# Kernel optimization log

Measured on AMD Instinct MI355X. Metric: run time of the kernel, lower is better.

Reference implementation:

```python
import jax, jax.numpy as jnp
import numpy as np

W = 16          # hidden width
N_HIDDEN = 8    # number of 16->16 hidden layers (num_layers - 1)
N_PTS = 2097152


def setup_inputs() -> dict:
    key = jax.random.key(0)
    ks = jax.random.split(key, 7)
    x = jax.random.uniform(ks[0], (N_PTS, 3), dtype=jnp.float32) * 2.0 - 1.0
    # nn.init.normal_ -> std-normal weights; biases left at (small) values
    W0 = jax.random.normal(ks[1], (W, 3), dtype=jnp.float32)
    b0 = jnp.zeros((W,), dtype=jnp.float32)
    Wh = jax.random.normal(ks[2], (N_HIDDEN, W, W), dtype=jnp.float32)
    bh = jnp.zeros((N_HIDDEN, W), dtype=jnp.float32)
    Wo = jax.random.normal(ks[3], (1, W), dtype=jnp.float32)
    bo = jnp.zeros((1,), dtype=jnp.float32)
    return {"x": x, "W0": W0, "b0": b0, "Wh": Wh, "bh": bh, "Wo": Wo, "bo": bo}


def reference(x, W0, b0, Wh, bh, Wo, bo):
    # Linear(3,16) + tanh
    h = jnp.tanh(x @ W0.T + b0)                     # [N, 16]
    def step(h, wb):
        w, b = wb
        return jnp.tanh(h @ w.T + b), None
    h, _ = jax.lax.scan(step, h, (Wh, bh))
    # Linear(16,1) + sigmoid
    return jax.nn.sigmoid(h @ Wo.T + bo)            # [N, 1]
```

## Files before the change

kernel.cpp:

```cpp
#include <hip/hip_runtime.h>

typedef __attribute__((ext_vector_type(4))) _Float16 half4;
typedef __attribute__((ext_vector_type(8))) _Float16 half8;
typedef __attribute__((ext_vector_type(4))) float floatx4;
typedef __attribute__((ext_vector_type(4))) unsigned uint4v;

#define NH 8
#define CHUNKS 8

struct Split2 { unsigned hi, lo; };

__device__ __forceinline__ Split2 split2(float t0, float t1) {
    unsigned hp = __builtin_bit_cast(unsigned, __builtin_amdgcn_cvt_pkrtz(t0, t1));
    float h0 = (float)__builtin_bit_cast(_Float16, (unsigned short)(hp & 0xffffu));
    float h1 = (float)__builtin_bit_cast(_Float16, (unsigned short)(hp >> 16));
    float l0 = (t0 - h0) * 2048.0f;
    float l1 = (t1 - h1) * 2048.0f;
    Split2 r;
    r.hi = hp;
    r.lo = __builtin_bit_cast(unsigned, __builtin_amdgcn_cvt_pkrtz(l0, l1));
    return r;
}

__device__ __forceinline__ floatx4 quad_r(float s0, float s1, float s2, float s3) {
    s0 = fminf(s0, 25.0f); s1 = fminf(s1, 25.0f);
    s2 = fminf(s2, 25.0f); s3 = fminf(s3, 25.0f);
    float p0 = __builtin_amdgcn_exp2f(s0) + 1.0f;
    float p1 = __builtin_amdgcn_exp2f(s1) + 1.0f;
    float p2 = __builtin_amdgcn_exp2f(s2) + 1.0f;
    float p3 = __builtin_amdgcn_exp2f(s3) + 1.0f;
    float A = p0 * p1, B = p2 * p3;
    float P = A * B;
    float rp = __builtin_amdgcn_rcpf(P);
    float rA = rp * B, rB = rp * A;
    floatx4 r;
    r[0] = rA * p1; r[1] = rA * p0; r[2] = rB * p3; r[3] = rB * p2;
    return r;
}

__device__ __forceinline__ void split_w(float w, float& hi, float& lo) {
    _Float16 h = (_Float16)w;
    hi = (float)h;
    lo = (w - hi) * 2048.0f;
}

__device__ __forceinline__ half8 mk_frag(floatx4 rq) {
    Split2 p01 = split2(rq[0], rq[1]);
    Split2 p23 = split2(rq[2], rq[3]);
    uint4v hb;
    hb.x = p01.hi; hb.y = p23.hi;
    hb.z = p01.lo; hb.w = p23.lo;
    return __builtin_bit_cast(half8, hb);
}

__global__ __launch_bounds__(256, 4) void cppn_kernel(
    const float* __restrict__ x,
    const float* __restrict__ W0,
    const float* __restrict__ b0,
    const float* __restrict__ Wh,
    const float* __restrict__ bh,
    const float* __restrict__ Wo,
    const float* __restrict__ bo,
    float* __restrict__ out)
{
    const int tid  = threadIdx.x;
    const int lane = tid & 63;
    const int col  = lane & 15;
    const int kg   = lane >> 4;
    const int wib  = tid >> 6;

    const float TSCL = 2.8853900817779268f;
    const float NSCL = -2.0f * TSCL;
    const float OSCL = -1.4426950408889634f;
    const float UNSC = 4.8828125e-4f;

    half8   wA8[NH];
    floatx4 bC[NH];
    #pragma unroll
    for (int l = 0; l < NH; ++l) {
        const float* wrow = Wh + l*256 + col*16 + kg*4;
        float w0 = wrow[0], w1 = wrow[1], w2 = wrow[2], w3 = wrow[3];
        float rs = (w0 + w1) + (w2 + w3);
        rs += __shfl_xor(rs, 16);
        rs += __shfl_xor(rs, 32);
        float h0,h1,h2,h3, lo0,lo1,lo2,lo3;
        split_w(w0*NSCL, h0, lo0);
        split_w(w1*NSCL, h1, lo1);
        split_w(w2*NSCL, h2, lo2);
        split_w(w3*NSCL, h3, lo3);
        uint4v wa;
        wa.x = __builtin_bit_cast(unsigned, __builtin_amdgcn_cvt_pkrtz(lo0, lo1));
        wa.y = __builtin_bit_cast(unsigned, __builtin_amdgcn_cvt_pkrtz(lo2, lo3));
        wa.z = __builtin_bit_cast(unsigned, __builtin_amdgcn_cvt_pkrtz(h0, h1));
        wa.w = __builtin_bit_cast(unsigned, __builtin_amdgcn_cvt_pkrtz(h2, h3));
        wA8[l] = __builtin_bit_cast(half8, wa);
        floatx4 c;
        #pragma unroll
        for (int r = 0; r < 4; ++r) {
            float rs_r = __shfl(rs, kg*4 + r);
            c[r] = TSCL * (bh[l*16 + kg*4 + r] + rs_r);
        }
        bC[l] = c;
    }

    float w0r[4][3]; float b0r[4];
    #pragma unroll
    for (int r = 0; r < 4; ++r) {
        const float* wp = W0 + (kg*4 + r)*3;
        w0r[r][0] = wp[0]*TSCL; w0r[r][1] = wp[1]*TSCL; w0r[r][2] = wp[2]*TSCL;
        b0r[r] = b0[kg*4 + r]*TSCL;
    }

    float woP[4];
    float wsum;
    {
        const float* wp = Wo + kg*4;
        float a = wp[0], b = wp[1], c2 = wp[2], d = wp[3];
        wsum = (a + b) + (c2 + d);
        wsum += __shfl_xor(wsum, 16);
        wsum += __shfl_xor(wsum, 32);
        woP[0] = a*(-2.0f*OSCL); woP[1] = b*(-2.0f*OSCL);
        woP[2] = c2*(-2.0f*OSCL); woP[3] = d*(-2.0f*OSCL);
    }
    const float boP = OSCL * (bo[0] + wsum);

    const floatx4 zeroC = {0.0f, 0.0f, 0.0f, 0.0f};
    const int base0 = (blockIdx.x * 4 + wib) * (64 * CHUNKS);

    #pragma unroll 1
    for (int c = 0; c < CHUNKS; ++c) {
        const int base = base0 + c * 64;

        half8 hB[4];
        #pragma unroll
        for (int t = 0; t < 4; ++t) {
            const int p = base + t*16 + col;
            const float x0 = x[p*3+0], x1 = x[p*3+1], x2 = x[p*3+2];
            float a0 = fmaf(w0r[0][0],x0, fmaf(w0r[0][1],x1, fmaf(w0r[0][2],x2, b0r[0])));
            float a1 = fmaf(w0r[1][0],x0, fmaf(w0r[1][1],x1, fmaf(w0r[1][2],x2, b0r[1])));
            float a2 = fmaf(w0r[2][0],x0, fmaf(w0r[2][1],x1, fmaf(w0r[2][2],x2, b0r[2])));
            float a3 = fmaf(w0r[3][0],x0, fmaf(w0r[3][1],x1, fmaf(w0r[3][2],x2, b0r[3])));
            hB[t] = mk_frag(quad_r(a0, a1, a2, a3));
        }

        #pragma unroll
        for (int l = 0; l < NH-1; ++l) {
            const half8 wa8 = wA8[l];
            const half4 whi = __builtin_shufflevector(wa8, wa8, 4, 5, 6, 7);
            const floatx4 bc = bC[l];
            #pragma unroll
            for (int tp = 0; tp < 2; ++tp) {
                const int u0 = tp*2, u1 = tp*2+1;
                const half4 bhi0 = __builtin_shufflevector(hB[u0], hB[u0], 0, 1, 2, 3);
                const half4 bhi1 = __builtin_shufflevector(hB[u1], hB[u1], 0, 1, 2, 3);
                floatx4 d0 = __builtin_amdgcn_mfma_f32_16x16x16f16(whi, bhi0, bc, 0,0,0);
                floatx4 d1 = __builtin_amdgcn_mfma_f32_16x16x16f16(whi, bhi1, bc, 0,0,0);
                floatx4 e0 = __builtin_amdgcn_mfma_f32_16x16x32_f16(wa8, hB[u0], zeroC, 0,0,0);
                floatx4 e1 = __builtin_amdgcn_mfma_f32_16x16x32_f16(wa8, hB[u1], zeroC, 0,0,0);

                floatx4 q0 = quad_r(fmaf(e0[0], UNSC, d0[0]),
                                    fmaf(e0[1], UNSC, d0[1]),
                                    fmaf(e0[2], UNSC, d0[2]),
                                    fmaf(e0[3], UNSC, d0[3]));
                floatx4 q1 = quad_r(fmaf(e1[0], UNSC, d1[0]),
                                    fmaf(e1[1], UNSC, d1[1]),
                                    fmaf(e1[2], UNSC, d1[2]),
                                    fmaf(e1[3], UNSC, d1[3]));
                hB[u0] = mk_frag(q0);
                hB[u1] = mk_frag(q1);
            }
        }

        float tot[4];
        {
            const half8 wa8 = wA8[NH-1];
            const half4 whi = __builtin_shufflevector(wa8, wa8, 4, 5, 6, 7);
            const floatx4 bc = bC[NH-1];
            #pragma unroll
            for (int t = 0; t < 4; ++t) {
                const half4 bhi = __builtin_shufflevector(hB[t], hB[t], 0, 1, 2, 3);
                floatx4 d = __builtin_amdgcn_mfma_f32_16x16x16f16(whi, bhi, bc, 0,0,0);
                floatx4 e = __builtin_amdgcn_mfma_f32_16x16x32_f16(wa8, hB[t], zeroC, 0,0,0);
                floatx4 r8 = quad_r(fmaf(e[0], UNSC, d[0]),
                                    fmaf(e[1], UNSC, d[1]),
                                    fmaf(e[2], UNSC, d[2]),
                                    fmaf(e[3], UNSC, d[3]));
                float acc = fmaf(woP[0], r8[0],
                            fmaf(woP[1], r8[1],
                            fmaf(woP[2], r8[2], woP[3] * r8[3])));
                acc += __shfl_xor(acc, 16);
                acc += __shfl_xor(acc, 32);
                tot[t] = acc;
            }
        }

        float s = (kg == 0) ? tot[0] : (kg == 1) ? tot[1] : (kg == 2) ? tot[2] : tot[3];
        s += boP;
        float E = __builtin_amdgcn_exp2f(s);
        out[base + lane] = __builtin_amdgcn_rcpf(1.0f + E);
    }
}

extern "C" void kernel_launch(void* const* d_in, const int* in_sizes, int n_in,
                              void* d_out, int out_size, void* d_ws, size_t ws_size,
                              hipStream_t stream) {
    const float* x  = (const float*)d_in[0];
    const float* W0 = (const float*)d_in[1];
    const float* b0 = (const float*)d_in[2];
    const float* Wh = (const float*)d_in[3];
    const float* bh = (const float*)d_in[4];
    const float* Wo = (const float*)d_in[5];
    const float* bo = (const float*)d_in[6];
    float* out = (float*)d_out;

    int n = out_size;
    int block = 256;
    long ptsPerBlock = 4L * 64 * CHUNKS;
    int grid = (int)((n + ptsPerBlock - 1) / ptsPerBlock);
    cppn_kernel<<<grid, block, 0, stream>>>(x, W0, b0, Wh, bh, Wo, bo, out);
}
```

Before: 109.1 us.

## Stage preprocessed weights in LDS and cap VGPRs to raise occupancy

Result: faster. 100.2 us (-8.2%).

```diff
diff --git a/kernel.cpp b/kernel.cpp
--- a/kernel.cpp
+++ b/kernel.cpp
@@ -6,7 +6,7 @@
 typedef __attribute__((ext_vector_type(4))) unsigned uint4v;
 
 #define NH 8
-#define CHUNKS 8
+#define CHUNKS 4
 
 struct Split2 { unsigned hi, lo; };
 
@@ -53,7 +53,11 @@
     return __builtin_bit_cast(half8, hb);
 }
 
-__global__ __launch_bounds__(256, 4) void cppn_kernel(
+__global__ __launch_bounds__(256)
+#if __has_attribute(amdgpu_num_vgpr)
+__attribute__((amdgpu_num_vgpr(60)))
+#endif
+void cppn_kernel(
     const float* __restrict__ x,
     const float* __restrict__ W0,
     const float* __restrict__ b0,
@@ -63,6 +67,12 @@
     const float* __restrict__ bo,
     float* __restrict__ out)
 {
+    __shared__ uint4v  s_wA[NH][64];
+    __shared__ floatx4 s_bC[NH][4];
+    __shared__ floatx4 s_w0[4][4];
+    __shared__ floatx4 s_wo4[4];
+    __shared__ float   s_boP;
+
     const int tid  = threadIdx.x;
     const int lane = tid & 63;
     const int col  = lane & 15;
@@ -74,55 +84,52 @@
     const float OSCL = -1.4426950408889634f;
     const float UNSC = 4.8828125e-4f;
 
-    half8   wA8[NH];
-    floatx4 bC[NH];
-    #pragma unroll
-    for (int l = 0; l < NH; ++l) {
-        const float* wrow = Wh + l*256 + col*16 + kg*4;
-        float w0 = wrow[0], w1 = wrow[1], w2 = wrow[2], w3 = wrow[3];
-        float rs = (w0 + w1) + (w2 + w3);
-        rs += __shfl_xor(rs, 16);
-        rs += __shfl_xor(rs, 32);
-        float h0,h1,h2,h3, lo0,lo1,lo2,lo3;
-        split_w(w0*NSCL, h0, lo0);
-        split_w(w1*NSCL, h1, lo1);
-        split_w(w2*NSCL, h2, lo2);
-        split_w(w3*NSCL, h3, lo3);
-        uint4v wa;
-        wa.x = __builtin_bit_cast(unsigned, __builtin_amdgcn_cvt_pkrtz(lo0, lo1));
-        wa.y = __builtin_bit_cast(unsigned, __builtin_amdgcn_cvt_pkrtz(lo2, lo3));
-        wa.z = __builtin_bit_cast(unsigned, __builtin_amdgcn_cvt_pkrtz(h0, h1));
-        wa.w = __builtin_bit_cast(unsigned, __builtin_amdgcn_cvt_pkrtz(h2, h3));
-        wA8[l] = __builtin_bit_cast(half8, wa);
-        floatx4 c;
-        #pragma unroll
-        for (int r = 0; r < 4; ++r) {
-            float rs_r = __shfl(rs, kg*4 + r);
-            c[r] = TSCL * (bh[l*16 + kg*4 + r] + rs_r);
-        }
-        bC[l] = c;
+    if (tid < 64) {
+        #pragma unroll
+        for (int l = 0; l < NH; ++l) {
+            const float* wrow = Wh + l*256 + col*16 + kg*4;
+            float w0v = wrow[0], w1v = wrow[1], w2v = wrow[2], w3v = wrow[3];
+            float rs = (w0v + w1v) + (w2v + w3v);
+            rs += __shfl_xor(rs, 16);
+            rs += __shfl_xor(rs, 32);
+            float h0,h1,h2,h3, lo0,lo1,lo2,lo3;
+            split_w(w0v*NSCL, h0, lo0);
+            split_w(w1v*NSCL, h1, lo1);
+            split_w(w2v*NSCL, h2, lo2);
+            split_w(w3v*NSCL, h3, lo3);
+            uint4v wa;
+            wa.x = __builtin_bit_cast(unsigned, __builtin_amdgcn_cvt_pkrtz(lo0, lo1));
+            wa.y = __builtin_bit_cast(unsigned, __builtin_amdgcn_cvt_pkrtz(lo2, lo3));
+            wa.z = __builtin_bit_cast(unsigned, __builtin_amdgcn_cvt_pkrtz(h0, h1));
+            wa.w = __builtin_bit_cast(unsigned, __builtin_amdgcn_cvt_pkrtz(h2, h3));
+            s_wA[l][tid] = wa;
+            floatx4 c;
+            #pragma unroll
+            for (int r = 0; r < 4; ++r) {
+                float rs_r = __shfl(rs, kg*4 + r);
+                c[r] = TSCL * (bh[l*16 + kg*4 + r] + rs_r);
+            }
+            if (col == 0) s_bC[l][kg] = c;
+        }
+    } else if (tid < 80) {
+        const int t = tid - 64, r = t & 3, g = t >> 2, row = g*4 + r;
+        floatx4 v;
+        v[0] = W0[row*3+0]*TSCL; v[1] = W0[row*3+1]*TSCL;
+        v[2] = W0[row*3+2]*TSCL; v[3] = b0[row]*TSCL;
+        s_w0[r][g] = v;
+    } else if (tid < 84) {
+        const int g = tid - 80;
+        floatx4 v;
+        v[0] = Wo[g*4+0]*(-2.0f*OSCL); v[1] = Wo[g*4+1]*(-2.0f*OSCL);
+        v[2] = Wo[g*4+2]*(-2.0f*OSCL); v[3] = Wo[g*4+3]*(-2.0f*OSCL);
+        s_wo4[g] = v;
+    } else if (tid == 84) {
+        float ws = 0.0f;
+        #pragma unroll
+        for (int i = 0; i < 16; ++i) ws += Wo[i];
+        s_boP = OSCL * (bo[0] + ws);
     }
-
-    float w0r[4][3]; float b0r[4];
-    #pragma unroll
-    for (int r = 0; r < 4; ++r) {
-        const float* wp = W0 + (kg*4 + r)*3;
-        w0r[r][0] = wp[0]*TSCL; w0r[r][1] = wp[1]*TSCL; w0r[r][2] = wp[2]*TSCL;
-        b0r[r] = b0[kg*4 + r]*TSCL;
-    }
-
-    float woP[4];
-    float wsum;
-    {
-        const float* wp = Wo + kg*4;
-        float a = wp[0], b = wp[1], c2 = wp[2], d = wp[3];
-        wsum = (a + b) + (c2 + d);
-        wsum += __shfl_xor(wsum, 16);
-        wsum += __shfl_xor(wsum, 32);
-        woP[0] = a*(-2.0f*OSCL); woP[1] = b*(-2.0f*OSCL);
-        woP[2] = c2*(-2.0f*OSCL); woP[3] = d*(-2.0f*OSCL);
-    }
-    const float boP = OSCL * (bo[0] + wsum);
+    __syncthreads();
 
     const floatx4 zeroC = {0.0f, 0.0f, 0.0f, 0.0f};
     const int base0 = (blockIdx.x * 4 + wib) * (64 * CHUNKS);
@@ -136,18 +143,20 @@
         for (int t = 0; t < 4; ++t) {
             const int p = base + t*16 + col;
             const float x0 = x[p*3+0], x1 = x[p*3+1], x2 = x[p*3+2];
-            float a0 = fmaf(w0r[0][0],x0, fmaf(w0r[0][1],x1, fmaf(w0r[0][2],x2, b0r[0])));
-            float a1 = fmaf(w0r[1][0],x0, fmaf(w0r[1][1],x1, fmaf(w0r[1][2],x2, b0r[1])));
-            float a2 = fmaf(w0r[2][0],x0, fmaf(w0r[2][1],x1, fmaf(w0r[2][2],x2, b0r[2])));
-            float a3 = fmaf(w0r[3][0],x0, fmaf(w0r[3][1],x1, fmaf(w0r[3][2],x2, b0r[3])));
+            const floatx4 w0v0 = s_w0[0][kg], w0v1 = s_w0[1][kg];
+            const floatx4 w0v2 = s_w0[2][kg], w0v3 = s_w0[3][kg];
+            float a0 = fmaf(w0v0[0],x0, fmaf(w0v0[1],x1, fmaf(w0v0[2],x2, w0v0[3])));
+            float a1 = fmaf(w0v1[0],x0, fmaf(w0v1[1],x1, fmaf(w0v1[2],x2, w0v1[3])));
+            float a2 = fmaf(w0v2[0],x0, fmaf(w0v2[1],x1, fmaf(w0v2[2],x2, w0v2[3])));
+            float a3 = fmaf(w0v3[0],x0, fmaf(w0v3[1],x1, fmaf(w0v3[2],x2, w0v3[3])));
             hB[t] = mk_frag(quad_r(a0, a1, a2, a3));
         }
 
         #pragma unroll
         for (int l = 0; l < NH-1; ++l) {
-            const half8 wa8 = wA8[l];
+            const half8 wa8 = __builtin_bit_cast(half8, s_wA[l][lane]);
             const half4 whi = __builtin_shufflevector(wa8, wa8, 4, 5, 6, 7);
-            const floatx4 bc = bC[l];
+            const floatx4 bc = s_bC[l][kg];
             #pragma unroll
             for (int tp = 0; tp < 2; ++tp) {
                 const int u0 = tp*2, u1 = tp*2+1;
@@ -173,9 +182,10 @@
 
         float tot[4];
         {
-            const half8 wa8 = wA8[NH-1];
+            const half8 wa8 = __builtin_bit_cast(half8, s_wA[NH-1][lane]);
             const half4 whi = __builtin_shufflevector(wa8, wa8, 4, 5, 6, 7);
-            const floatx4 bc = bC[NH-1];
+            const floatx4 bc = s_bC[NH-1][kg];
+            const floatx4 wov = s_wo4[kg];
             #pragma unroll
             for (int t = 0; t < 4; ++t) {
                 const half4 bhi = __builtin_shufflevector(hB[t], hB[t], 0, 1, 2, 3);
@@ -185,9 +195,9 @@
                                     fmaf(e[1], UNSC, d[1]),
                                     fmaf(e[2], UNSC, d[2]),
                                     fmaf(e[3], UNSC, d[3]));
-                float acc = fmaf(woP[0], r8[0],
-                            fmaf(woP[1], r8[1],
-                            fmaf(woP[2], r8[2], woP[3] * r8[3])));
+                float acc = fmaf(wov[0], r8[0],
+                            fmaf(wov[1], r8[1],
+                            fmaf(wov[2], r8[2], wov[3] * r8[3])));
                 acc += __shfl_xor(acc, 16);
                 acc += __shfl_xor(acc, 32);
                 tot[t] = acc;
@@ -195,7 +205,7 @@
         }
 
         float s = (kg == 0) ? tot[0] : (kg == 1) ? tot[1] : (kg == 2) ? tot[2] : tot[3];
-        s += boP;
+        s += s_boP;
         float E = __builtin_amdgcn_exp2f(s);
         out[base + lane] = __builtin_amdgcn_rcpf(1.0f + E);
     }
```
